# Kernel optimization log

Measured on AMD Instinct MI355X. Metric: run time of the kernel, lower is better.

## Reference

```python
import jax, jax.numpy as jnp
import numpy as np


def setup_inputs() -> dict:
    key = jax.random.key(0)
    ks = jax.random.split(key, 8)
    B, T, N = 8, 8192, 256
    x = jax.random.normal(ks[0], (B, T, N), dtype=jnp.float32)
    # stable-ish LRU params: nu_log/theta_log as in the torch init
    u1 = jax.random.uniform(ks[1], (N,), dtype=jnp.float32)
    r_min, r_max = 0.4, 0.9
    nu_log = jnp.log(-0.5 * jnp.log(u1 * (r_max + r_min) * (r_max - r_min) + r_min ** 2))
    u2 = jax.random.uniform(ks[2], (N,), dtype=jnp.float32)
    theta_log = jnp.log(2.0 * np.pi * u2)
    L_mod = jnp.exp(-jnp.exp(nu_log))
    gamma_log = jnp.log(jnp.sqrt(1.0 - jnp.square(L_mod)))
    s2 = 1.0 / np.sqrt(2 * N)
    s1 = 1.0 / np.sqrt(N)
    B_re = jax.random.normal(ks[3], (N, N), dtype=jnp.float32) * s2
    B_im = jax.random.normal(ks[4], (N, N), dtype=jnp.float32) * s2
    C_re = jax.random.normal(ks[5], (N, N), dtype=jnp.float32) * s1
    C_im = jax.random.normal(ks[6], (N, N), dtype=jnp.float32) * s1
    return {"x": x, "nu_log": nu_log, "theta_log": theta_log, "gamma_log": gamma_log,
            "B_re": B_re, "B_im": B_im, "C_re": C_re, "C_im": C_im}


def _binop(e_i, e_j):
    # associative combine for diagonal linear recurrence h_j = a_j * h_i + b_j
    a_i, b_i = e_i
    a_j, b_j = e_j
    return a_j * a_i, a_j * b_i + b_j


def reference(x, nu_log, theta_log, gamma_log, B_re, B_im, C_re, C_im):
    # Lambda (diagonal complex state transition)
    L_mod = jnp.exp(-jnp.exp(nu_log))                     # [N]
    theta = jnp.exp(theta_log)                            # [N]
    L_diag = (L_mod * jnp.cos(theta) + 1j * (L_mod * jnp.sin(theta)))  # complex64 [N]
    # normalized input projection
    B_norm = (B_re + 1j * B_im) * jnp.exp(gamma_log)[:, None]          # [N, N]
    Bu = jnp.einsum('btn,mn->btm', x.astype(B_norm.dtype), B_norm)     # [B, T, N] complex
    L_elems = jnp.broadcast_to(L_diag, Bu.shape)                        # [B, T, N]
    # parallel associative scan over time axis (zero initial state)
    _, states = jax.lax.associative_scan(_binop, (L_elems, Bu), axis=1)
    C = C_re + 1j * C_im
    return jnp.einsum('btn,mn->btm', states, C).real
```

## Files before the change

### kernel.cpp

```cpp
#include <hip/hip_runtime.h>

#define NB 8
#define TT 8192
#define NN 256
#define CH 64
#define BT (NB*TT)
#define NCHUNK (BT/CH)
#define GPB (TT/CH)

typedef float f4 __attribute__((ext_vector_type(4)));
typedef unsigned u4 __attribute__((ext_vector_type(4)));
typedef short b4 __attribute__((ext_vector_type(4)));
typedef short b8 __attribute__((ext_vector_type(8)));

static __device__ __forceinline__ ushort f2bf(float f) {
  union { float f; unsigned u; } v; v.f = f;
  return (ushort)((v.u + 0x7fffu + ((v.u >> 16) & 1u)) >> 16);
}
static __device__ __forceinline__ float bf2f(ushort h) {
  union { unsigned u; float f; } v; v.u = ((unsigned)h) << 16; return v.f;
}

__global__ void k_setup(const float* __restrict__ nu_log, const float* __restrict__ theta_log,
                        const float* __restrict__ gamma_log,
                        const float* __restrict__ B_re, const float* __restrict__ B_im,
                        const float* __restrict__ C_re, const float* __restrict__ C_im,
                        float2* __restrict__ Lc, float2* __restrict__ LCH,
                        float2* __restrict__ Lpow,
                        ushort* __restrict__ BnRe, ushort* __restrict__ BnIm,
                        ushort* __restrict__ CRe, ushort* __restrict__ CIm) {
  int bid = blockIdx.x, tid = threadIdx.x;
  if (bid < NN) {
    int m = bid, n = tid;
    float g = expf(gamma_log[m]);
    int idx = m * NN + n;
    BnRe[idx] = f2bf(B_re[idx] * g);
    BnIm[idx] = f2bf(B_im[idx] * g);
    CRe[idx]  = f2bf(C_re[idx]);
    CIm[idx]  = f2bf(-C_im[idx]);
  } else {
    int m = tid;
    float Lmod = expf(-expf(nu_log[m]));
    float th = expf(theta_log[m]);
    float lre = Lmod * cosf(th), lim = Lmod * sinf(th);
    Lc[m] = make_float2(lre, lim);
    float pr = 1.f, pi = 0.f;
    for (int k = 0; k < CH; ++k) {
      Lpow[(size_t)(CH - 1 - k) * NN + m] = make_float2(pr, pi);
      float npr = pr * lre - pi * lim;
      pi = pr * lim + pi * lre;
      pr = npr;
    }
    LCH[m] = make_float2(pr, pi);
  }
}

static __device__ __forceinline__ void stage_x_bf16(const float* __restrict__ xt,
                                                    char* lds, int tid) {
#pragma unroll
  for (int i = 0; i < 16; ++i) {
    int fi = i * 1024 + tid * 4;
    f4 w = *(const f4*)(xt + fi);
    int r = fi >> 8, c = fi & 255;
    int dst = r * 512 + ((c * 2) ^ ((r & 7) << 4));
    b4 p;
    p[0] = (short)f2bf(w[0]); p[1] = (short)f2bf(w[1]);
    p[2] = (short)f2bf(w[2]); p[3] = (short)f2bf(w[3]);
    *(b4*)(lds + dst) = p;
  }
}

static __device__ __forceinline__ void gemm1_ldsx(const char* lds,
                                                  const ushort* __restrict__ BnRe,
                                                  const ushort* __restrict__ BnIm,
                                                  int tid, f4 accRe[4][4], f4 accIm[4][4]) {
  int lane = tid & 63, wid = tid >> 6;
  int lr = lane & 15, lg = lane >> 4;
  int mq = wid * 64;
  for (int ks = 0; ks < 8; ++ks) {
    int k0 = ks * 32 + lg * 8;
    b8 a[4];
    for (int mf = 0; mf < 4; ++mf) {
      int r = mf * 16 + lr;
      a[mf] = *(const b8*)(lds + r * 512 + ((k0 * 2) ^ ((r & 7) << 4)));
    }
    for (int nf = 0; nf < 4; ++nf) {
      int mrow = mq + nf * 16 + lr;
      b8 br = *(const b8*)(BnRe + (size_t)mrow * NN + k0);
      b8 bi = *(const b8*)(BnIm + (size_t)mrow * NN + k0);
      for (int mf = 0; mf < 4; ++mf) {
        accRe[mf][nf] = __builtin_amdgcn_mfma_f32_16x16x32_bf16(a[mf], br, accRe[mf][nf], 0, 0, 0);
        accIm[mf][nf] = __builtin_amdgcn_mfma_f32_16x16x32_bf16(a[mf], bi, accIm[mf][nf], 0, 0, 0);
      }
    }
  }
}

__global__ __launch_bounds__(256) void k_carry(const float* __restrict__ x,
                                               const ushort* __restrict__ BnRe,
                                               const ushort* __restrict__ BnIm,
                                               const float2* __restrict__ Lc,
                                               const float2* __restrict__ Lpow,
                                               float2* __restrict__ carry) {
  __shared__ char lds[32768];
  int cid = blockIdx.x, tid = threadIdx.x;
  int lane = tid & 63, wid = tid >> 6;
  int lr = lane & 15, lg = lane >> 4;
  int mq = wid * 64;

  float2 pL1[4], pL4[4], pL8[4], pL16[4];
  for (int nf = 0; nf < 4; ++nf) {
    int c = mq + nf * 16 + lr;
    pL1[nf]  = Lc[c];
    pL4[nf]  = Lpow[(size_t)(CH - 1 - 4)  * NN + c];
    pL8[nf]  = Lpow[(size_t)(CH - 1 - 8)  * NN + c];
    pL16[nf] = Lpow[(size_t)(CH - 1 - 16) * NN + c];
  }

  stage_x_bf16(x + (size_t)cid * CH * NN, lds, tid);
  __syncthreads();

  f4 accRe[4][4], accIm[4][4];
  for (int i = 0; i < 4; ++i)
    for (int j = 0; j < 4; ++j) { accRe[i][j] = (f4)0.f; accIm[i][j] = (f4)0.f; }
  gemm1_ldsx(lds, BnRe, BnIm, tid, accRe, accIm);

  for (int nf = 0; nf < 4; ++nf) {
    float2 L1 = pL1[nf], L4 = pL4[nf], L8 = pL8[nf], L16 = pL16[nf];
    float Cr[4], Ci[4];
    for (int mf = 0; mf < 4; ++mf) {
      float cr = accRe[mf][nf][0], ci = accIm[mf][nf][0];
      for (int q = 1; q < 4; ++q) {
        float nr = L1.x * cr - L1.y * ci + accRe[mf][nf][q];
        ci = L1.x * ci + L1.y * cr + accIm[mf][nf][q];
        cr = nr;
      }
      Cr[mf] = cr; Ci[mf] = ci;
    }
    float Hx = 0.f, Hy = 0.f;
    for (int mf = 0; mf < 4; ++mf) {
      float tx = __shfl_up(Cr[mf], 16, 64), ty = __shfl_up(Ci[mf], 16, 64);
      float m1 = (lg >= 1) ? 1.f : 0.f;
      float ax = Cr[mf] + m1 * (L4.x * tx - L4.y * ty);
      float ay = Ci[mf] + m1 * (L4.x * ty + L4.y * tx);
      float ux = __shfl_up(ax, 32, 64), uy = __shfl_up(ay, 32, 64);
      float m2 = (lg >= 2) ? 1.f : 0.f;
      float Ix = ax + m2 * (L8.x * ux - L8.y * uy);
      float Iy = ay + m2 * (L8.x * uy + L8.y * ux);
      float Qx = __shfl(Ix, lr + 48, 64), Qy = __shfl(Iy, lr + 48, 64);
      float nHx = Qx + L16.x * Hx - L16.y * Hy;
      Hy = Qy + L16.x * Hy + L16.y * Hx;
      Hx = nHx;
    }
    if (lg == 0) carry[(size_t)cid * NN + mq + nf * 16 + lr] = make_float2(Hx, Hy);
  }
}

__global__ void k_seed(float2* __restrict__ carrySeed, const float2* __restrict__ LCH) {
  int b = blockIdx.x, m = threadIdx.x;
  float2 LC = LCH[m];
  float hr = 0.f, hi = 0.f;
  size_t base = (size_t)b * GPB * NN + m;
  for (int g0 = 0; g0 < GPB; g0 += 16) {
    float2 buf[16];
#pragma unroll
    for (int j = 0; j < 16; ++j)
      buf[j] = carrySeed[base + (size_t)(g0 + j) * NN];
#pragma unroll
    for (int j = 0; j < 16; ++j) {
      carrySeed[base + (size_t)(g0 + j) * NN] = make_float2(hr, hi);
      float2 c = buf[j];
      float nr = LC.x * hr - LC.y * hi + c.x;
      hi = LC.x * hi + LC.y * hr + c.y;
      hr = nr;
    }
  }
}

__global__ __launch_bounds__(256) void k_out(const float* __restrict__ x,
                                             const ushort* __restrict__ BnRe,
                                             const ushort* __restrict__ BnIm,
                                             const float2* __restrict__ Lc,
                                             const float2* __restrict__ seed,
                                             const ushort* __restrict__ CRe,
                                             const ushort* __restrict__ CIm,
                                             const float2* __restrict__ Lpow,
                                             float* __restrict__ out) {
  __shared__ char lds[65536];
  int cid = blockIdx.x, tid = threadIdx.x;
  size_t rowbase = (size_t)cid * CH;
  int lane = tid & 63, wid = tid >> 6;
  int lr = lane & 15, lg = lane >> 4;
  int mq = wid * 64;

  float2 pL1[4], pL4[4], pL8[4], pL16[4], pw4[4], psd[4];
  for (int nf = 0; nf < 4; ++nf) {
    int c = mq + nf * 16 + lr;
    pL1[nf]  = Lc[c];
    pL4[nf]  = Lpow[(size_t)(CH - 1 - 4)  * NN + c];
    pL8[nf]  = Lpow[(size_t)(CH - 1 - 8)  * NN + c];
    pL16[nf] = Lpow[(size_t)(CH - 1 - 16) * NN + c];
    pw4[nf]  = (lg == 0) ? make_float2(1.f, 0.f)
                         : Lpow[(size_t)(CH - 1 - 4 * lg) * NN + c];
    psd[nf]  = seed[(size_t)cid * NN + c];
  }

  stage_x_bf16(x + rowbase * NN, lds, tid);
  __syncthreads();

  f4 accRe[4][4], accIm[4][4];
  for (int i = 0; i < 4; ++i)
    for (int j = 0; j < 4; ++j) { accRe[i][j] = (f4)0.f; accIm[i][j] = (f4)0.f; }
  gemm1_ldsx(lds, BnRe, BnIm, tid, accRe, accIm);

  for (int nf = 0; nf < 4; ++nf) {
    float2 L1 = pL1[nf], L4 = pL4[nf], L8 = pL8[nf], L16 = pL16[nf];
    float2 w4 = pw4[nf], sd = psd[nf];

    float Cr[4], Ci[4];
    for (int mf = 0; mf < 4; ++mf) {
      for (int q = 1; q < 4; ++q) {
        float sr_ = L1.x * accRe[mf][nf][q-1] - L1.y * accIm[mf][nf][q-1] + accRe[mf][nf][q];
        float si_ = L1.x * accIm[mf][nf][q-1] + L1.y * accRe[mf][nf][q-1] + accIm[mf][nf][q];
        accRe[mf][nf][q] = sr_; accIm[mf][nf][q] = si_;
      }
      Cr[mf] = accRe[mf][nf][3]; Ci[mf] = accIm[mf][nf][3];
    }

    float Er[4], Ei[4], Qr[4], Qi[4];
    for (int mf = 0; mf < 4; ++mf) {
      float tx = __shfl_up(Cr[mf], 16, 64), ty = __shfl_up(Ci[mf], 16, 64);
      float m1 = (lg >= 1) ? 1.f : 0.f;
      float ax = Cr[mf] + m1 * (L4.x * tx - L4.y * ty);
      float ay = Ci[mf] + m1 * (L4.x * ty + L4.y * tx);
      float ux = __shfl_up(ax, 32, 64), uy = __shfl_up(ay, 32, 64);
      float m2 = (lg >= 2) ? 1.f : 0.f;
      float Ix = ax + m2 * (L8.x * ux - L8.y * uy);
      float Iy = ay + m2 * (L8.x * uy + L8.y * ux);
      float ex = __shfl_up(Ix, 16, 64), ey = __shfl_up(Iy, 16, 64);
      Er[mf] = m1 * ex; Ei[mf] = m1 * ey;
      Qr[mf] = __shfl(Ix, lr + 48, 64); Qi[mf] = __shfl(Iy, lr + 48, 64);
    }

    float Hx = sd.x, Hy = sd.y;
    for (int mf = 0; mf < 4; ++mf) {
      float Zx = Er[mf] + w4.x * Hx - w4.y * Hy;
      float Zy = Ei[mf] + w4.x * Hy + w4.y * Hx;
      float Wx = L1.x, Wy = L1.y;
      for (int q = 0; q < 4; ++q) {
        float hr_ = accRe[mf][nf][q] + Wx * Zx - Wy * Zy;
        float hi_ = accIm[mf][nf][q] + Wx * Zy + Wy * Zx;
        accRe[mf][nf][q] = hr_; accIm[mf][nf][q] = hi_;
        if (q < 3) { float nWx = Wx * L1.x - Wy * L1.y; Wy = Wx * L1.y + Wy * L1.x; Wx = nWx; }
      }
      float nHx = Qr[mf] + L16.x * Hx - L16.y * Hy;
      Hy = Qi[mf] + L16.x * Hy + L16.y * Hx;
      Hx = nHx;
    }
  }
  __syncthreads();

  for (int mf = 0; mf < 4; ++mf)
    for (int nf = 0; nf < 4; ++nf)
      for (int r = 0; r < 4; ++r) {
        int row = mf * 16 + lg * 4 + r;
        int col = mq + nf * 16 + lr;
        unsigned p = (unsigned)f2bf(accRe[mf][nf][r]) | ((unsigned)f2bf(accIm[mf][nf][r]) << 16);
        int off = row * 1024 + ((col * 4) ^ ((row & 7) << 4));
        *(unsigned*)(lds + off) = p;
      }
  __syncthreads();

  f4 acc[4][4];
  for (int i = 0; i < 4; ++i)
    for (int j = 0; j < 4; ++j) acc[i][j] = (f4)0.f;

  for (int ks = 0; ks < 8; ++ks) {
    int k0 = ks * 32 + lg * 8;
    b8 ar[4], ai[4];
    for (int mf = 0; mf < 4; ++mf) {
      int row = mf * 16 + lr;
      int m4 = (row & 7) << 4;
      const char* base = lds + row * 1024;
      u4 p0 = *(const u4*)(base + ((k0 * 4) ^ m4));
      u4 p1 = *(const u4*)(base + ((k0 * 4 + 16) ^ m4));
      b8 tr, ti;
      tr[0] = (short)(p0[0] & 0xffffu); ti[0] = (short)(p0[0] >> 16);
      tr[1] = (short)(p0[1] & 0xffffu); ti[1] = (short)(p0[1] >> 16);
      tr[2] = (short)(p0[2] & 0xffffu); ti[2] = (short)(p0[2] >> 16);
      tr[3] = (short)(p0[3] & 0xffffu); ti[3] = (short)(p0[3] >> 16);
      tr[4] = (short)(p1[0] & 0xffffu); ti[4] = (short)(p1[0] >> 16);
      tr[5] = (short)(p1[1] & 0xffffu); ti[5] = (short)(p1[1] >> 16);
      tr[6] = (short)(p1[2] & 0xffffu); ti[6] = (short)(p1[2] >> 16);
      tr[7] = (short)(p1[3] & 0xffffu); ti[7] = (short)(p1[3] >> 16);
      ar[mf] = tr; ai[mf] = ti;
    }
    for (int nf = 0; nf < 4; ++nf) {
      int m = mq + nf * 16 + lr;
      b8 cr = *(const b8*)(CRe + (size_t)m * NN + k0);
      b8 ci = *(const b8*)(CIm + (size_t)m * NN + k0);
      for (int mf = 0; mf < 4; ++mf) {
        acc[mf][nf] = __builtin_amdgcn_mfma_f32_16x16x32_bf16(ar[mf], cr, acc[mf][nf], 0, 0, 0);
        acc[mf][nf] = __builtin_amdgcn_mfma_f32_16x16x32_bf16(ai[mf], ci, acc[mf][nf], 0, 0, 0);
      }
    }
  }
  for (int mf = 0; mf < 4; ++mf)
    for (int nf = 0; nf < 4; ++nf)
      for (int r = 0; r < 4; ++r) {
        size_t t = rowbase + mf * 16 + lg * 4 + r;
        out[t * NN + mq + nf * 16 + lr] = acc[mf][nf][r];
      }
}

extern "C" void kernel_launch(void* const* d_in, const int* in_sizes, int n_in,
                              void* d_out, int out_size, void* d_ws, size_t ws_size,
                              hipStream_t stream) {
  const float* x         = (const float*)d_in[0];
  const float* nu_log    = (const float*)d_in[1];
  const float* theta_log = (const float*)d_in[2];
  const float* gamma_log = (const float*)d_in[3];
  const float* B_re      = (const float*)d_in[4];
  const float* B_im      = (const float*)d_in[5];
  const float* C_re      = (const float*)d_in[6];
  const float* C_im      = (const float*)d_in[7];
  float* out = (float*)d_out;

  char* ws = (char*)d_ws;
  float2*  carrySeed = (float2*)(ws + 0);
  float2*  Lc   = (float2*)(ws + 2097152);
  float2*  LCH  = (float2*)(ws + 2099200);
  ushort*  BnRe = (ushort*)(ws + 2101248);
  ushort*  BnIm = (ushort*)(ws + 2232320);
  ushort*  CRe  = (ushort*)(ws + 2363392);
  ushort*  CIm  = (ushort*)(ws + 2494464);
  float2*  Lpow = (float2*)(ws + 2625536);

  hipLaunchKernelGGL(k_setup, dim3(NN + 1), dim3(NN), 0, stream,
                     nu_log, theta_log, gamma_log, B_re, B_im, C_re, C_im,
                     Lc, LCH, Lpow, BnRe, BnIm, CRe, CIm);
  hipLaunchKernelGGL(k_carry, dim3(NCHUNK), dim3(256), 0, stream,
                     x, BnRe, BnIm, Lc, Lpow, carrySeed);
  hipLaunchKernelGGL(k_seed, dim3(NB), dim3(NN), 0, stream, carrySeed, LCH);
  hipLaunchKernelGGL(k_out, dim3(NCHUNK), dim3(256), 0, stream,
                     x, BnRe, BnIm, Lc, carrySeed, CRe, CIm, Lpow, out);
}
```

Measured before the change: 181.5 us.

## Pre-swizzle weights into MFMA fragment order and split output GEMM into halves

The setup kernel now stores the bf16 B and C weight matrices in a fragment-major layout, so each lane's 8-element MFMA operand is one contiguous 16-byte load and a wave's loads are fully coalesced. The output kernel stages the hidden states to LDS in two 32-row halves instead of all 64 rows, which halves LDS use (64KB to 32KB) to allow more resident blocks and lowers the register footprint of the second GEMM. The cost is extra barriers and reloading the C fragments twice per block.

```diff
diff --git a/kernel.cpp b/kernel.cpp
--- a/kernel.cpp
+++ b/kernel.cpp
@@ -34,10 +34,12 @@
     int m = bid, n = tid;
     float g = expf(gamma_log[m]);
     int idx = m * NN + n;
-    BnRe[idx] = f2bf(B_re[idx] * g);
-    BnIm[idx] = f2bf(B_im[idx] * g);
-    CRe[idx]  = f2bf(C_re[idx]);
-    CIm[idx]  = f2bf(-C_im[idx]);
+    int fidx = ((((m >> 6) * 8 + (n >> 5)) * 4 + ((m >> 4) & 3)) * 64
+                + (((n >> 3) & 3) * 16 + (m & 15))) * 8 + (n & 7);
+    BnRe[fidx] = f2bf(B_re[idx] * g);
+    BnIm[fidx] = f2bf(B_im[idx] * g);
+    CRe[fidx]  = f2bf(C_re[idx]);
+    CIm[fidx]  = f2bf(-C_im[idx]);
   } else {
     int m = tid;
     float Lmod = expf(-expf(nu_log[m]));
@@ -70,13 +72,12 @@
   }
 }
 
-static __device__ __forceinline__ void gemm1_ldsx(const char* lds,
-                                                  const ushort* __restrict__ BnRe,
-                                                  const ushort* __restrict__ BnIm,
-                                                  int tid, f4 accRe[4][4], f4 accIm[4][4]) {
+static __device__ __forceinline__ void gemm1_ldsx_bf(const char* lds,
+                                                     const ushort* __restrict__ BnRe,
+                                                     const ushort* __restrict__ BnIm,
+                                                     int tid, f4 accRe[4][4], f4 accIm[4][4]) {
   int lane = tid & 63, wid = tid >> 6;
   int lr = lane & 15, lg = lane >> 4;
-  int mq = wid * 64;
   for (int ks = 0; ks < 8; ++ks) {
     int k0 = ks * 32 + lg * 8;
     b8 a[4];
@@ -85,15 +86,33 @@
       a[mf] = *(const b8*)(lds + r * 512 + ((k0 * 2) ^ ((r & 7) << 4)));
     }
     for (int nf = 0; nf < 4; ++nf) {
-      int mrow = mq + nf * 16 + lr;
-      b8 br = *(const b8*)(BnRe + (size_t)mrow * NN + k0);
-      b8 bi = *(const b8*)(BnIm + (size_t)mrow * NN + k0);
+      int fb = (((wid * 8 + ks) * 4 + nf) << 9) + (lane << 3);
+      b8 br = *(const b8*)(BnRe + fb);
+      b8 bi = *(const b8*)(BnIm + fb);
       for (int mf = 0; mf < 4; ++mf) {
         accRe[mf][nf] = __builtin_amdgcn_mfma_f32_16x16x32_bf16(a[mf], br, accRe[mf][nf], 0, 0, 0);
         accIm[mf][nf] = __builtin_amdgcn_mfma_f32_16x16x32_bf16(a[mf], bi, accIm[mf][nf], 0, 0, 0);
       }
     }
   }
+}
+
+static __device__ __forceinline__ void ld_h_frag(const char* lds, int rowl, int k0,
+                                                 b8* tr_, b8* ti_) {
+  int m4 = (rowl & 7) << 4;
+  const char* base = lds + rowl * 1024;
+  u4 p0 = *(const u4*)(base + ((k0 * 4) ^ m4));
+  u4 p1 = *(const u4*)(base + ((k0 * 4 + 16) ^ m4));
+  b8 tr, ti;
+  tr[0] = (short)(p0[0] & 0xffffu); ti[0] = (short)(p0[0] >> 16);
+  tr[1] = (short)(p0[1] & 0xffffu); ti[1] = (short)(p0[1] >> 16);
+  tr[2] = (short)(p0[2] & 0xffffu); ti[2] = (short)(p0[2] >> 16);
+  tr[3] = (short)(p0[3] & 0xffffu); ti[3] = (short)(p0[3] >> 16);
+  tr[4] = (short)(p1[0] & 0xffffu); ti[4] = (short)(p1[0] >> 16);
+  tr[5] = (short)(p1[1] & 0xffffu); ti[5] = (short)(p1[1] >> 16);
+  tr[6] = (short)(p1[2] & 0xffffu); ti[6] = (short)(p1[2] >> 16);
+  tr[7] = (short)(p1[3] & 0xffffu); ti[7] = (short)(p1[3] >> 16);
+  *tr_ = tr; *ti_ = ti;
 }
 
 __global__ __launch_bounds__(256) void k_carry(const float* __restrict__ x,
@@ -123,7 +142,7 @@
   f4 accRe[4][4], accIm[4][4];
   for (int i = 0; i < 4; ++i)
     for (int j = 0; j < 4; ++j) { accRe[i][j] = (f4)0.f; accIm[i][j] = (f4)0.f; }
-  gemm1_ldsx(lds, BnRe, BnIm, tid, accRe, accIm);
+  gemm1_ldsx_bf(lds, BnRe, BnIm, tid, accRe, accIm);
 
   for (int nf = 0; nf < 4; ++nf) {
     float2 L1 = pL1[nf], L4 = pL4[nf], L8 = pL8[nf], L16 = pL16[nf];
@@ -177,6 +196,48 @@
   }
 }
 
+#define GEMM2_HALF(MFA, MFB, ROWOFF)                                              \
+  {                                                                               \
+    __syncthreads();                                                              \
+    for (int nf = 0; nf < 4; ++nf)                                                \
+      for (int r = 0; r < 4; ++r) {                                               \
+        int col = mq + nf * 16 + lr;                                              \
+        int rowl = lg * 4 + r;                                                    \
+        unsigned p = (unsigned)f2bf(accRe[MFA][nf][r]) |                          \
+                     ((unsigned)f2bf(accIm[MFA][nf][r]) << 16);                   \
+        *(unsigned*)(lds + rowl * 1024 + ((col * 4) ^ ((rowl & 7) << 4))) = p;    \
+        rowl = 16 + lg * 4 + r;                                                   \
+        p = (unsigned)f2bf(accRe[MFB][nf][r]) |                                   \
+            ((unsigned)f2bf(accIm[MFB][nf][r]) << 16);                            \
+        *(unsigned*)(lds + rowl * 1024 + ((col * 4) ^ ((rowl & 7) << 4))) = p;    \
+      }                                                                           \
+    __syncthreads();                                                              \
+    f4 acc0[4], acc1[4];                                                          \
+    for (int j = 0; j < 4; ++j) { acc0[j] = (f4)0.f; acc1[j] = (f4)0.f; }         \
+    for (int ks = 0; ks < 8; ++ks) {                                              \
+      int k0 = ks * 32 + lg * 8;                                                  \
+      b8 ar0, ai0, ar1, ai1;                                                      \
+      ld_h_frag(lds, lr, k0, &ar0, &ai0);                                         \
+      ld_h_frag(lds, 16 + lr, k0, &ar1, &ai1);                                    \
+      for (int nf = 0; nf < 4; ++nf) {                                            \
+        int fb = (((wid * 8 + ks) * 4 + nf) << 9) + (lane << 3);                  \
+        b8 cr = *(const b8*)(CRe + fb);                                           \
+        b8 ci = *(const b8*)(CIm + fb);                                           \
+        acc0[nf] = __builtin_amdgcn_mfma_f32_16x16x32_bf16(ar0, cr, acc0[nf], 0, 0, 0); \
+        acc0[nf] = __builtin_amdgcn_mfma_f32_16x16x32_bf16(ai0, ci, acc0[nf], 0, 0, 0); \
+        acc1[nf] = __builtin_amdgcn_mfma_f32_16x16x32_bf16(ar1, cr, acc1[nf], 0, 0, 0); \
+        acc1[nf] = __builtin_amdgcn_mfma_f32_16x16x32_bf16(ai1, ci, acc1[nf], 0, 0, 0); \
+      }                                                                           \
+    }                                                                             \
+    for (int nf = 0; nf < 4; ++nf)                                                \
+      for (int r = 0; r < 4; ++r) {                                               \
+        size_t t0 = rowbase + (ROWOFF) + lg * 4 + r;                              \
+        out[t0 * NN + mq + nf * 16 + lr] = acc0[nf][r];                           \
+        size_t t1 = rowbase + (ROWOFF) + 16 + lg * 4 + r;                         \
+        out[t1 * NN + mq + nf * 16 + lr] = acc1[nf][r];                           \
+      }                                                                           \
+  }
+
 __global__ __launch_bounds__(256) void k_out(const float* __restrict__ x,
                                              const ushort* __restrict__ BnRe,
                                              const ushort* __restrict__ BnIm,
@@ -186,7 +247,7 @@
                                              const ushort* __restrict__ CIm,
                                              const float2* __restrict__ Lpow,
                                              float* __restrict__ out) {
-  __shared__ char lds[65536];
+  __shared__ char lds[32768];
   int cid = blockIdx.x, tid = threadIdx.x;
   size_t rowbase = (size_t)cid * CH;
   int lane = tid & 63, wid = tid >> 6;
@@ -211,7 +272,7 @@
   f4 accRe[4][4], accIm[4][4];
   for (int i = 0; i < 4; ++i)
     for (int j = 0; j < 4; ++j) { accRe[i][j] = (f4)0.f; accIm[i][j] = (f4)0.f; }
-  gemm1_ldsx(lds, BnRe, BnIm, tid, accRe, accIm);
+  gemm1_ldsx_bf(lds, BnRe, BnIm, tid, accRe, accIm);
 
   for (int nf = 0; nf < 4; ++nf) {
     float2 L1 = pL1[nf], L4 = pL4[nf], L8 = pL8[nf], L16 = pL16[nf];
@@ -258,59 +319,9 @@
       Hx = nHx;
     }
   }
-  __syncthreads();
-
-  for (int mf = 0; mf < 4; ++mf)
-    for (int nf = 0; nf < 4; ++nf)
-      for (int r = 0; r < 4; ++r) {
-        int row = mf * 16 + lg * 4 + r;
-        int col = mq + nf * 16 + lr;
-        unsigned p = (unsigned)f2bf(accRe[mf][nf][r]) | ((unsigned)f2bf(accIm[mf][nf][r]) << 16);
-        int off = row * 1024 + ((col * 4) ^ ((row & 7) << 4));
-        *(unsigned*)(lds + off) = p;
-      }
-  __syncthreads();
-
-  f4 acc[4][4];
-  for (int i = 0; i < 4; ++i)
-    for (int j = 0; j < 4; ++j) acc[i][j] = (f4)0.f;
-
-  for (int ks = 0; ks < 8; ++ks) {
-    int k0 = ks * 32 + lg * 8;
-    b8 ar[4], ai[4];
-    for (int mf = 0; mf < 4; ++mf) {
-      int row = mf * 16 + lr;
-      int m4 = (row & 7) << 4;
-      const char* base = lds + row * 1024;
-      u4 p0 = *(const u4*)(base + ((k0 * 4) ^ m4));
-      u4 p1 = *(const u4*)(base + ((k0 * 4 + 16) ^ m4));
-      b8 tr, ti;
-      tr[0] = (short)(p0[0] & 0xffffu); ti[0] = (short)(p0[0] >> 16);
-      tr[1] = (short)(p0[1] & 0xffffu); ti[1] = (short)(p0[1] >> 16);
-      tr[2] = (short)(p0[2] & 0xffffu); ti[2] = (short)(p0[2] >> 16);
-      tr[3] = (short)(p0[3] & 0xffffu); ti[3] = (short)(p0[3] >> 16);
-      tr[4] = (short)(p1[0] & 0xffffu); ti[4] = (short)(p1[0] >> 16);
-      tr[5] = (short)(p1[1] & 0xffffu); ti[5] = (short)(p1[1] >> 16);
-      tr[6] = (short)(p1[2] & 0xffffu); ti[6] = (short)(p1[2] >> 16);
-      tr[7] = (short)(p1[3] & 0xffffu); ti[7] = (short)(p1[3] >> 16);
-      ar[mf] = tr; ai[mf] = ti;
-    }
-    for (int nf = 0; nf < 4; ++nf) {
-      int m = mq + nf * 16 + lr;
-      b8 cr = *(const b8*)(CRe + (size_t)m * NN + k0);
-      b8 ci = *(const b8*)(CIm + (size_t)m * NN + k0);
-      for (int mf = 0; mf < 4; ++mf) {
-        acc[mf][nf] = __builtin_amdgcn_mfma_f32_16x16x32_bf16(ar[mf], cr, acc[mf][nf], 0, 0, 0);
-        acc[mf][nf] = __builtin_amdgcn_mfma_f32_16x16x32_bf16(ai[mf], ci, acc[mf][nf], 0, 0, 0);
-      }
-    }
-  }
-  for (int mf = 0; mf < 4; ++mf)
-    for (int nf = 0; nf < 4; ++nf)
-      for (int r = 0; r < 4; ++r) {
-        size_t t = rowbase + mf * 16 + lg * 4 + r;
-        out[t * NN + mq + nf * 16 + lr] = acc[mf][nf][r];
-      }
+
+  GEMM2_HALF(0, 1, 0)
+  GEMM2_HALF(2, 3, 32)
 }
 
 extern "C" void kernel_launch(void* const* d_in, const int* in_sizes, int n_in,
```

Measured after the change: 171.5 us. 5.5% less time.
